# Optimization experiments

Hardware: AMD Instinct MI355X
Metric: run time of the kernel (lower is better)

Reference implementation:

```python
import jax, jax.numpy as jnp
import numpy as np

GRID = (8192, 8192)   # 2D lattice, *dims
NDIM = 2              # links.shape[0]
P_LINK = 0.45         # subcritical bond probability -> finite clusters, bounded step count


def setup_inputs() -> dict:
    key = jax.random.key(0)
    k1, k2 = jax.random.split(key)
    # links[i] marks an open bond between site x and its +1 neighbour along axis i
    links = jax.random.uniform(k1, (NDIM,) + GRID) < P_LINK
    seed_idx = jax.random.randint(k2, (NDIM,), 0, GRID[0]).astype(jnp.int32)
    return {"links": links, "seed_idx": seed_idx}


def _flood_fill(links, seed_idx):
    """Faithful port of ClusterSelection.from_seed_idx: BFS-style roll+mask
    expansion iterated to fixed point via lax.while_loop."""
    ndim = links.shape[0]
    grid = links.shape[1:]
    selected0 = jnp.zeros(grid, dtype=bool).at[tuple(seed_idx)].set(True)

    def cond(carry):
        _, is_done, _ = carry
        return ~is_done

    def body(carry):
        sel0, _, steps = carry
        sel = sel0
        for i in range(ndim):  # unrolled over the (small, static) ndim
            # sites whose -1-neighbour or self is selected can use bond i
            links_to_try = sel0 | jnp.roll(sel0, -1, i)
            links_sel = links_to_try & links[i]
            # a taken bond marks both of its endpoints
            links_sel = links_sel | jnp.roll(links_sel, 1, i)
            sel = sel | links_sel
        is_done = (sel ^ sel0).sum() == 0
        return sel, is_done, steps + 1

    sel, _, steps = jax.lax.while_loop(
        cond, body, (selected0, jnp.array(False), jnp.array(0, jnp.int32))
    )
    return sel, steps


def reference(links, seed_idx):
    sel, _steps = _flood_fill(links, seed_idx)
    return sel
```

## Files before the change

kernel.cpp:

```cpp
#include <hip/hip_runtime.h>
#include <stdint.h>

#define GW 8192
#define GMASK 8191
#define PLANE 67108864ULL
#define TPD 128
#define TMASK 127
#define NTILES 16384
#define QCAP 8192
#define WPR 128

typedef unsigned long long u64;
typedef unsigned int u32;

__global__ void clear_bitmap_kernel(uint4* __restrict__ p, int n) {
    int i = blockIdx.x * blockDim.x + threadIdx.x;
    if (i < n) p[i] = make_uint4(0, 0, 0, 0);
}

__global__ void detect_fmt_kernel(const unsigned char* __restrict__ links, int* __restrict__ flag) {
    __shared__ int c1, c3;
    if (threadIdx.x == 0) { c1 = 0; c3 = 0; }
    __syncthreads();
    int l1 = 0, l3 = 0;
    for (int i = threadIdx.x; i < 16384; i += blockDim.x) {
        if (links[i]) {
            int m = i & 3;
            if (m == 1) l1++;
            else if (m == 3) l3++;
        }
    }
    atomicAdd(&c1, l1);
    atomicAdd(&c3, l3);
    __syncthreads();
    if (threadIdx.x == 0) *flag = (c1 > 0) ? 0 : ((c3 > 0) ? 2 : 1);
}

__device__ __forceinline__ u32 nib4(u32 w) {
    return (((w & 0x01010101u) * 0x01020408u) >> 24) & 0xFu;
}
__device__ __forceinline__ u64 pack_row_b8(const unsigned char* p) {
    const uint4* q = (const uint4*)p;
    u64 w = 0;
#pragma unroll
    for (int i = 0; i < 4; i++) {
        uint4 v = q[i];
        u64 nb = (u64)(nib4(v.x) | (nib4(v.y) << 4) | (nib4(v.z) << 8) | (nib4(v.w) << 12));
        w |= nb << (16 * i);
    }
    return w;
}
__device__ __forceinline__ u64 pack_row_b32(const u32* p) {
    u64 w = 0;
#pragma unroll
    for (int k = 0; k < 16; k++) {
        uint4 v = ((const uint4*)p)[k];
        u64 nb = (u64)((v.x != 0) | ((v.y != 0) << 1) | ((v.z != 0) << 2) | ((v.w != 0) << 3));
        w |= nb << (4 * k);
    }
    return w;
}

__global__ void __launch_bounds__(1024)
bfs_tiles_kernel(const unsigned char* __restrict__ links8,
                 const int* __restrict__ seed_idx,
                 u64* __restrict__ bitmap,
                 const int* __restrict__ flag) {
    __shared__ unsigned short q[2][QCAP];
    __shared__ u32 tflags[NTILES / 32];
    __shared__ int s_cnt, s_ncnt, s_head, s_flip, s_mode;

    const int tid = threadIdx.x;
    const int ln  = tid & 63;

    for (int i = tid; i < NTILES / 32; i += 1024) tflags[i] = 0;
    if (tid == 0) {
        s_mode = *flag;
        int sr = seed_idx[0] & GMASK, sc = seed_idx[1] & GMASK;
        atomicOr(&bitmap[(u64)sr * WPR + (sc >> 6)], 1ull << (sc & 63));
        int t = (sr >> 6) * TPD + (sc >> 6);
        tflags[t >> 5] = 1u << (t & 31);
        q[0][0] = (unsigned short)t;
        s_cnt = 1; s_ncnt = 0; s_head = 0; s_flip = 0;
    }
    __syncthreads();

    const int mode = s_mode;
    const unsigned char* p0b = links8;
    const unsigned char* p1b = links8 + PLANE;
    const u32* p0w = (const u32*)links8;
    const u32* p1w = (const u32*)(links8 + PLANE * 4);

    int safety = 0;
    while (true) {
        const int flip = s_flip;
        const int cnt  = s_cnt;

        auto enq = [&](int t) {
            u32 bit = 1u << (t & 31);
            u32 old = atomicOr(&tflags[t >> 5], bit);
            if (!(old & bit)) {
                int p = atomicAdd(&s_ncnt, 1);
                if (p < QCAP) q[flip ^ 1][p] = (unsigned short)t;
            }
        };

        while (true) {
            int pos = 0;
            if (ln == 0) pos = atomicAdd(&s_head, 1);
            pos = __shfl(pos, 0);
            if (pos >= cnt) break;
            int t = q[flip][pos];
            int tR = t >> 7, tC = t & TMASK;
            if (ln == 0) atomicAnd(&tflags[t >> 5], ~(1u << (t & 31)));
            __threadfence_block();

            const int gr = tR * 64 + ln;
            u64* wp = &bitmap[(u64)gr * WPR + tC];
            u64 loaded = *(volatile u64*)wp;

            u64 l0, l1;
            if (mode == 0) {
                l0 = pack_row_b8(p0b + (u64)gr * GW + tC * 64);
                l1 = pack_row_b8(p1b + (u64)gr * GW + tC * 64);
            } else {
                l0 = pack_row_b32(p0w + (u64)gr * GW + tC * 64);
                l1 = pack_row_b32(p1w + (u64)gr * GW + tC * 64);
            }

            u64 sel = loaded;
            while (true) {
                u64 old = sel;
                sel |= (sel & l1) << 1;
                sel |= (sel >> 1) & l1;
                u64 sb = sel & l0;
                u64 up = __shfl_up(sb, 1);
                if (ln > 0) sel |= up;
                u64 dn = __shfl_down(sel, 1);
                if (ln < 63) sel |= dn & l0;
                if (__ballot(sel != old) == 0ull) break;
            }

            u64 newbits = sel & ~loaded;
            if (newbits) atomicOr(wp, newbits);

            const int c0 = tC * 64;
            bool rnew = false, lnew = false;
            if ((sel >> 63) & (l1 >> 63) & 1ull) {
                u64 old = atomicOr(&bitmap[(u64)gr * WPR + ((tC + 1) & TMASK)], 1ull);
                rnew = !(old & 1ull);
            }
            {
                u64 lcol = (u64)((c0 - 1) & GMASK);
                bool lopen = (mode == 0) ? (p1b[(u64)gr * GW + lcol] != 0)
                                         : (p1w[(u64)gr * GW + lcol] != 0);
                if ((sel & 1ull) && lopen) {
                    u64 old = atomicOr(&bitmap[(u64)gr * WPR + ((tC - 1) & TMASK)], 1ull << 63);
                    lnew = !(old & (1ull << 63));
                }
            }
            u64 rmask = __ballot(rnew), lmask = __ballot(lnew);

            const int ga = (tR * 64 - 1) & GMASK;
            bool bopen = (mode == 0) ? (p0b[(u64)ga * GW + c0 + ln] != 0)
                                     : (p0w[(u64)ga * GW + c0 + ln] != 0);
            u64 top_sel = __shfl(sel, 0);
            u64 umask = __ballot(bopen && ((top_sel >> ln) & 1));
            u64 unew = 0;
            if (ln == 0 && umask) {
                u64 old = atomicOr(&bitmap[(u64)ga * WPR + tC], umask);
                unew = umask & ~old;
            }
            u64 dmask = sel & l0;
            const int gb = (tR * 64 + 64) & GMASK;
            u64 dnew = 0;
            if (ln == 63 && dmask) {
                u64 old = atomicOr(&bitmap[(u64)gb * WPR + tC], dmask);
                dnew = dmask & ~old;
            }

            if (ln == 0  && rmask) enq(tR * TPD + ((tC + 1) & TMASK));
            if (ln == 1  && lmask) enq(tR * TPD + ((tC - 1) & TMASK));
            if (ln == 0  && unew)  enq(((tR - 1) & TMASK) * TPD + tC);
            if (ln == 63 && dnew)  enq(((tR + 1) & TMASK) * TPD + tC);
        }

        __syncthreads();
        if (tid == 0) { s_cnt = s_ncnt; s_ncnt = 0; s_head = 0; s_flip ^= 1; }
        __syncthreads();
        if (s_cnt == 0) break;
        if (++safety > 30000) break;
    }
}

__global__ void writeout_kernel(const u64* __restrict__ bitmap, int4* __restrict__ out) {
    int g = blockIdx.x * blockDim.x + threadIdx.x;
    int site0 = g << 2;
    u64 w = bitmap[site0 >> 6];
    u32 b = (u32)(w >> (site0 & 63)) & 0xFu;
    out[g] = make_int4(b & 1, (b >> 1) & 1, (b >> 2) & 1, (b >> 3) & 1);
}

extern "C" void kernel_launch(void* const* d_in, const int* in_sizes, int n_in,
                              void* d_out, int out_size, void* d_ws, size_t ws_size,
                              hipStream_t stream) {
    const unsigned char* links = (const unsigned char*)d_in[0];
    const int* seed = (const int*)d_in[1];

    int* flag   = (int*)d_ws;
    u64* bitmap = (u64*)((char*)d_ws + 4096);

    clear_bitmap_kernel<<<2048, 256, 0, stream>>>((uint4*)bitmap, 524288);
    detect_fmt_kernel<<<1, 256, 0, stream>>>(links, flag);
    bfs_tiles_kernel<<<1, 1024, 0, stream>>>(links, seed, bitmap, flag);
    writeout_kernel<<<65536, 256, 0, stream>>>(bitmap, (int4*)d_out);
}
```

Baseline: 683.0 us.

## Replace level-synchronous tile BFS with async work queue and doubling intra-tile propagation

Replaces the double-buffered frontier queue and its block-wide barriers with a single circular shared-memory work queue. Wavefronts pop tiles via CAS and spin on sentinel slots, so they no longer wait for each other at every BFS level. The intra-tile fixed-point loop now uses precomputed doubling masks for runs of open bonds along rows and columns, so each iteration propagates up to 64 sites instead of one. The format-detection kernel is folded into the BFS kernel, removing one launch. The cost is extra atomics and spin-waits on shared counters, and a risk of livelock or of ending early if the active-count bookkeeping races.

Result: faster. 661.6 us (-3.1%).

```diff
diff --git a/kernel.cpp b/kernel.cpp
--- a/kernel.cpp
+++ b/kernel.cpp
@@ -7,7 +7,8 @@
 #define TPD 128
 #define TMASK 127
 #define NTILES 16384
-#define QCAP 8192
+#define QCAP 16384
+#define QMASK 16383
 #define WPR 128
 
 typedef unsigned long long u64;
@@ -16,24 +17,6 @@
 __global__ void clear_bitmap_kernel(uint4* __restrict__ p, int n) {
     int i = blockIdx.x * blockDim.x + threadIdx.x;
     if (i < n) p[i] = make_uint4(0, 0, 0, 0);
-}
-
-__global__ void detect_fmt_kernel(const unsigned char* __restrict__ links, int* __restrict__ flag) {
-    __shared__ int c1, c3;
-    if (threadIdx.x == 0) { c1 = 0; c3 = 0; }
-    __syncthreads();
-    int l1 = 0, l3 = 0;
-    for (int i = threadIdx.x; i < 16384; i += blockDim.x) {
-        if (links[i]) {
-            int m = i & 3;
-            if (m == 1) l1++;
-            else if (m == 3) l3++;
-        }
-    }
-    atomicAdd(&c1, l1);
-    atomicAdd(&c3, l3);
-    __syncthreads();
-    if (threadIdx.x == 0) *flag = (c1 > 0) ? 0 : ((c3 > 0) ? 2 : 1);
 }
 
 __device__ __forceinline__ u32 nib4(u32 w) {
@@ -64,24 +47,34 @@
 __global__ void __launch_bounds__(1024)
 bfs_tiles_kernel(const unsigned char* __restrict__ links8,
                  const int* __restrict__ seed_idx,
-                 u64* __restrict__ bitmap,
-                 const int* __restrict__ flag) {
-    __shared__ unsigned short q[2][QCAP];
+                 u64* __restrict__ bitmap) {
+    volatile __shared__ unsigned short q[QCAP];
     __shared__ u32 tflags[NTILES / 32];
-    __shared__ int s_cnt, s_ncnt, s_head, s_flip, s_mode;
+    __shared__ int s_qhead, s_qtail, s_active, s_mode, s_c1, s_c3;
 
     const int tid = threadIdx.x;
     const int ln  = tid & 63;
 
+    for (int i = tid; i < QCAP; i += 1024) q[i] = 0xFFFF;
     for (int i = tid; i < NTILES / 32; i += 1024) tflags[i] = 0;
+    if (tid == 0) { s_c1 = 0; s_c3 = 0; s_qhead = 0; s_qtail = 0; s_active = 0; }
+    __syncthreads();
+
+    int l1c = 0, l3c = 0;
+    for (int i = tid; i < 16384; i += 1024) {
+        if (links8[i]) { int m = i & 3; if (m == 1) l1c++; else if (m == 3) l3c++; }
+    }
+    atomicAdd(&s_c1, l1c);
+    atomicAdd(&s_c3, l3c);
+    __syncthreads();
     if (tid == 0) {
-        s_mode = *flag;
+        s_mode = (s_c1 > 0) ? 0 : ((s_c3 > 0) ? 2 : 1);
         int sr = seed_idx[0] & GMASK, sc = seed_idx[1] & GMASK;
         atomicOr(&bitmap[(u64)sr * WPR + (sc >> 6)], 1ull << (sc & 63));
         int t = (sr >> 6) * TPD + (sc >> 6);
         tflags[t >> 5] = 1u << (t & 31);
-        q[0][0] = (unsigned short)t;
-        s_cnt = 1; s_ncnt = 0; s_head = 0; s_flip = 0;
+        q[0] = (unsigned short)t;
+        s_qtail = 1; s_active = 1;
     }
     __syncthreads();
 
@@ -91,105 +84,131 @@
     const u32* p0w = (const u32*)links8;
     const u32* p1w = (const u32*)(links8 + PLANE * 4);
 
-    int safety = 0;
+    auto enq = [&](int t2) {
+        u32 bit = 1u << (t2 & 31);
+        u32 old = atomicOr(&tflags[t2 >> 5], bit);
+        if (!(old & bit)) {
+            atomicAdd(&s_active, 1);
+            int pos = atomicAdd(&s_qtail, 1) & QMASK;
+            q[pos] = (unsigned short)t2;
+        }
+    };
+
+    long long guard = 0;
     while (true) {
-        const int flip = s_flip;
-        const int cnt  = s_cnt;
-
-        auto enq = [&](int t) {
-            u32 bit = 1u << (t & 31);
-            u32 old = atomicOr(&tflags[t >> 5], bit);
-            if (!(old & bit)) {
-                int p = atomicAdd(&s_ncnt, 1);
-                if (p < QCAP) q[flip ^ 1][p] = (unsigned short)t;
+        int t = -1;
+        if (ln == 0) {
+            while (true) {
+                if (atomicAdd(&s_active, 0) == 0) break;
+                int h  = atomicAdd(&s_qhead, 0);
+                int tl = atomicAdd(&s_qtail, 0);
+                if (h != tl && atomicCAS(&s_qhead, h, h + 1) == h) {
+                    int pos = h & QMASK;
+                    unsigned short v;
+                    long long g2 = 0;
+                    while ((v = q[pos]) == 0xFFFF) { if (++g2 > 400000000LL) break; }
+                    q[pos] = 0xFFFF;
+                    t = v;
+                    break;
+                }
+                if (++guard > 400000000LL) break;
             }
-        };
-
+        }
+        t = __shfl(t, 0);
+        if (t < 0) break;
+
+        const int tR = t >> 7, tC = t & TMASK;
+        if (ln == 0) atomicAnd(&tflags[t >> 5], ~(1u << (t & 31)));
+        __threadfence_block();
+
+        const int gr = tR * 64 + ln;
+        u64* wp = &bitmap[(u64)gr * WPR + tC];
+        u64 loaded = *(volatile u64*)wp;
+
+        u64 l0, l1;
+        if (mode == 0) {
+            l0 = pack_row_b8(p0b + (u64)gr * GW + tC * 64);
+            l1 = pack_row_b8(p1b + (u64)gr * GW + tC * 64);
+        } else {
+            l0 = pack_row_b32(p0w + (u64)gr * GW + tC * 64);
+            l1 = pack_row_b32(p1w + (u64)gr * GW + tC * 64);
+        }
+
+        u64 P0 = l1 & 0x7FFFFFFFFFFFFFFFull;
+        u64 P1 = P0 & (P0 >> 1);
+        u64 P2 = P1 & (P1 >> 2);
+        u64 P3 = P2 & (P2 >> 4);
+        u64 P4 = P3 & (P3 >> 8);
+        u64 P5 = P4 & (P4 >> 16);
+        u64 D0 = (ln < 63) ? l0 : 0ull;
+        u64 D1 = D0 & __shfl_down(D0, 1);
+        u64 D2 = D1 & __shfl_down(D1, 2);
+        u64 D3 = D2 & __shfl_down(D2, 4);
+        u64 D4 = D3 & __shfl_down(D3, 8);
+        u64 D5 = D4 & __shfl_down(D4, 16);
+
+        u64 sel = loaded;
         while (true) {
-            int pos = 0;
-            if (ln == 0) pos = atomicAdd(&s_head, 1);
-            pos = __shfl(pos, 0);
-            if (pos >= cnt) break;
-            int t = q[flip][pos];
-            int tR = t >> 7, tC = t & TMASK;
-            if (ln == 0) atomicAnd(&tflags[t >> 5], ~(1u << (t & 31)));
-            __threadfence_block();
-
-            const int gr = tR * 64 + ln;
-            u64* wp = &bitmap[(u64)gr * WPR + tC];
-            u64 loaded = *(volatile u64*)wp;
-
-            u64 l0, l1;
-            if (mode == 0) {
-                l0 = pack_row_b8(p0b + (u64)gr * GW + tC * 64);
-                l1 = pack_row_b8(p1b + (u64)gr * GW + tC * 64);
-            } else {
-                l0 = pack_row_b32(p0w + (u64)gr * GW + tC * 64);
-                l1 = pack_row_b32(p1w + (u64)gr * GW + tC * 64);
+            u64 old = sel;
+            sel |= (sel & P0) << 1;  sel |= (sel >> 1)  & P0;
+            sel |= (sel & P1) << 2;  sel |= (sel >> 2)  & P1;
+            sel |= (sel & P2) << 4;  sel |= (sel >> 4)  & P2;
+            sel |= (sel & P3) << 8;  sel |= (sel >> 8)  & P3;
+            sel |= (sel & P4) << 16; sel |= (sel >> 16) & P4;
+            sel |= (sel & P5) << 32; sel |= (sel >> 32) & P5;
+            sel |= __shfl_up(sel & D0, 1);  sel |= __shfl_down(sel, 1)  & D0;
+            sel |= __shfl_up(sel & D1, 2);  sel |= __shfl_down(sel, 2)  & D1;
+            sel |= __shfl_up(sel & D2, 4);  sel |= __shfl_down(sel, 4)  & D2;
+            sel |= __shfl_up(sel & D3, 8);  sel |= __shfl_down(sel, 8)  & D3;
+            sel |= __shfl_up(sel & D4, 16); sel |= __shfl_down(sel, 16) & D4;
+            sel |= __shfl_up(sel & D5, 32); sel |= __shfl_down(sel, 32) & D5;
+            if (__ballot(sel != old) == 0ull) break;
+        }
+
+        u64 newbits = sel & ~loaded;
+        if (newbits) atomicOr(wp, newbits);
+
+        const int c0 = tC * 64;
+        bool rnew = false, lnew = false;
+        if ((sel >> 63) & (l1 >> 63) & 1ull) {
+            u64 old = atomicOr(&bitmap[(u64)gr * WPR + ((tC + 1) & TMASK)], 1ull);
+            rnew = !(old & 1ull);
+        }
+        {
+            u64 lcol = (u64)((c0 - 1) & GMASK);
+            bool lopen = (mode == 0) ? (p1b[(u64)gr * GW + lcol] != 0)
+                                     : (p1w[(u64)gr * GW + lcol] != 0);
+            if ((sel & 1ull) && lopen) {
+                u64 old = atomicOr(&bitmap[(u64)gr * WPR + ((tC - 1) & TMASK)], 1ull << 63);
+                lnew = !(old & (1ull << 63));
             }
-
-            u64 sel = loaded;
-            while (true) {
-                u64 old = sel;
-                sel |= (sel & l1) << 1;
-                sel |= (sel >> 1) & l1;
-                u64 sb = sel & l0;
-                u64 up = __shfl_up(sb, 1);
-                if (ln > 0) sel |= up;
-                u64 dn = __shfl_down(sel, 1);
-                if (ln < 63) sel |= dn & l0;
-                if (__ballot(sel != old) == 0ull) break;
-            }
-
-            u64 newbits = sel & ~loaded;
-            if (newbits) atomicOr(wp, newbits);
-
-            const int c0 = tC * 64;
-            bool rnew = false, lnew = false;
-            if ((sel >> 63) & (l1 >> 63) & 1ull) {
-                u64 old = atomicOr(&bitmap[(u64)gr * WPR + ((tC + 1) & TMASK)], 1ull);
-                rnew = !(old & 1ull);
-            }
-            {
-                u64 lcol = (u64)((c0 - 1) & GMASK);
-                bool lopen = (mode == 0) ? (p1b[(u64)gr * GW + lcol] != 0)
-                                         : (p1w[(u64)gr * GW + lcol] != 0);
-                if ((sel & 1ull) && lopen) {
-                    u64 old = atomicOr(&bitmap[(u64)gr * WPR + ((tC - 1) & TMASK)], 1ull << 63);
-                    lnew = !(old & (1ull << 63));
-                }
-            }
-            u64 rmask = __ballot(rnew), lmask = __ballot(lnew);
-
-            const int ga = (tR * 64 - 1) & GMASK;
-            bool bopen = (mode == 0) ? (p0b[(u64)ga * GW + c0 + ln] != 0)
-                                     : (p0w[(u64)ga * GW + c0 + ln] != 0);
-            u64 top_sel = __shfl(sel, 0);
-            u64 umask = __ballot(bopen && ((top_sel >> ln) & 1));
-            u64 unew = 0;
-            if (ln == 0 && umask) {
-                u64 old = atomicOr(&bitmap[(u64)ga * WPR + tC], umask);
-                unew = umask & ~old;
-            }
-            u64 dmask = sel & l0;
-            const int gb = (tR * 64 + 64) & GMASK;
-            u64 dnew = 0;
-            if (ln == 63 && dmask) {
-                u64 old = atomicOr(&bitmap[(u64)gb * WPR + tC], dmask);
-                dnew = dmask & ~old;
-            }
-
-            if (ln == 0  && rmask) enq(tR * TPD + ((tC + 1) & TMASK));
-            if (ln == 1  && lmask) enq(tR * TPD + ((tC - 1) & TMASK));
-            if (ln == 0  && unew)  enq(((tR - 1) & TMASK) * TPD + tC);
-            if (ln == 63 && dnew)  enq(((tR + 1) & TMASK) * TPD + tC);
-        }
-
-        __syncthreads();
-        if (tid == 0) { s_cnt = s_ncnt; s_ncnt = 0; s_head = 0; s_flip ^= 1; }
-        __syncthreads();
-        if (s_cnt == 0) break;
-        if (++safety > 30000) break;
+        }
+        u64 rmask = __ballot(rnew), lmask = __ballot(lnew);
+
+        const int ga = (tR * 64 - 1) & GMASK;
+        bool bopen = (mode == 0) ? (p0b[(u64)ga * GW + c0 + ln] != 0)
+                                 : (p0w[(u64)ga * GW + c0 + ln] != 0);
+        u64 top_sel = __shfl(sel, 0);
+        u64 umask = __ballot(bopen && ((top_sel >> ln) & 1));
+        u64 unew = 0;
+        if (ln == 0 && umask) {
+            u64 old = atomicOr(&bitmap[(u64)ga * WPR + tC], umask);
+            unew = umask & ~old;
+        }
+        u64 dmask = sel & l0;
+        const int gb = (tR * 64 + 64) & GMASK;
+        u64 dnew = 0;
+        if (ln == 63 && dmask) {
+            u64 old = atomicOr(&bitmap[(u64)gb * WPR + tC], dmask);
+            dnew = dmask & ~old;
+        }
+
+        if (ln == 0  && rmask) enq(tR * TPD + ((tC + 1) & TMASK));
+        if (ln == 1  && lmask) enq(tR * TPD + ((tC - 1) & TMASK));
+        if (ln == 0  && unew)  enq(((tR - 1) & TMASK) * TPD + tC);
+        if (ln == 63 && dnew)  enq(((tR + 1) & TMASK) * TPD + tC);
+
+        if (ln == 0) atomicSub(&s_active, 1);
     }
 }
 
@@ -207,11 +226,9 @@
     const unsigned char* links = (const unsigned char*)d_in[0];
     const int* seed = (const int*)d_in[1];
 
-    int* flag   = (int*)d_ws;
     u64* bitmap = (u64*)((char*)d_ws + 4096);
 
     clear_bitmap_kernel<<<2048, 256, 0, stream>>>((uint4*)bitmap, 524288);
-    detect_fmt_kernel<<<1, 256, 0, stream>>>(links, flag);
-    bfs_tiles_kernel<<<1, 1024, 0, stream>>>(links, seed, bitmap, flag);
+    bfs_tiles_kernel<<<1, 1024, 0, stream>>>(links, seed, bitmap);
     writeout_kernel<<<65536, 256, 0, stream>>>(bitmap, (int4*)d_out);
 }
```
